# Kernel tuning notes

Measured on AMD Instinct MI355X. Metric: run time of the kernel, lower is better.

Reference implementation:

```python
import jax, jax.numpy as jnp
import numpy as np

# constants from init_kwargs
NUM_ITERS = 3
NUM_SLOTS = 8
INPUT_SIZE = 64
SLOT_SIZE = 64
MLP_HIDDEN = 128
EPS = 1e-8
NUM_HEADS = 4
HEAD_DIM = SLOT_SIZE // NUM_HEADS

B = 64
N_KV = 8192


def layernorm(x, g, b):
    m = jnp.mean(x, axis=-1, keepdims=True)
    v = jnp.mean((x - m) ** 2, axis=-1, keepdims=True)
    return (x - m) * jax.lax.rsqrt(v + 1e-5) * g + b


def setup_inputs() -> dict:
    key = jax.random.key(0)
    ks = jax.random.split(key, 16)
    s = 0.02
    return {
        "inputs": jax.random.normal(ks[0], (B, N_KV, INPUT_SIZE), jnp.float32),
        "slots": jax.random.normal(ks[1], (B, NUM_SLOTS, SLOT_SIZE), jnp.float32),
        "ln_in_g": jnp.ones((INPUT_SIZE,), jnp.float32),
        "ln_in_b": jnp.zeros((INPUT_SIZE,), jnp.float32),
        "ln_slot_g": jnp.ones((SLOT_SIZE,), jnp.float32),
        "ln_slot_b": jnp.zeros((SLOT_SIZE,), jnp.float32),
        "ln_mlp_g": jnp.ones((SLOT_SIZE,), jnp.float32),
        "ln_mlp_b": jnp.zeros((SLOT_SIZE,), jnp.float32),
        "Wq": jax.random.normal(ks[2], (SLOT_SIZE, SLOT_SIZE), jnp.float32) * s,
        "Wk": jax.random.normal(ks[3], (INPUT_SIZE, SLOT_SIZE), jnp.float32) * s,
        "Wv": jax.random.normal(ks[4], (INPUT_SIZE, SLOT_SIZE), jnp.float32) * s,
        "W_ih": jax.random.normal(ks[5], (3 * SLOT_SIZE, SLOT_SIZE), jnp.float32) * s,
        "W_hh": jax.random.normal(ks[6], (3 * SLOT_SIZE, SLOT_SIZE), jnp.float32) * s,
        "b_ih": jnp.zeros((3 * SLOT_SIZE,), jnp.float32),
        "b_hh": jnp.zeros((3 * SLOT_SIZE,), jnp.float32),
        "mlp_W1": jax.random.normal(ks[7], (SLOT_SIZE, MLP_HIDDEN), jnp.float32) * s,
        "mlp_b1": jnp.zeros((MLP_HIDDEN,), jnp.float32),
        "mlp_W2": jax.random.normal(ks[8], (MLP_HIDDEN, SLOT_SIZE), jnp.float32) * s,
        "mlp_b2": jnp.zeros((SLOT_SIZE,), jnp.float32),
    }


def gru_cell(x, h, W_ih, W_hh, b_ih, b_hh):
    # torch.nn.GRUCell math
    gx = x @ W_ih.T + b_ih  # [..., 3D]
    gh = h @ W_hh.T + b_hh
    xr, xz, xn = jnp.split(gx, 3, axis=-1)
    hr, hz, hn = jnp.split(gh, 3, axis=-1)
    r = jax.nn.sigmoid(xr + hr)
    z = jax.nn.sigmoid(xz + hz)
    n = jnp.tanh(xn + r * hn)
    return (1.0 - z) * n + z * h


def reference(inputs, slots, ln_in_g, ln_in_b, ln_slot_g, ln_slot_b, ln_mlp_g, ln_mlp_b,
              Wq, Wk, Wv, W_ih, W_hh, b_ih, b_hh, mlp_W1, mlp_b1, mlp_W2, mlp_b2):
    b, n_kv, _ = inputs.shape
    n_q = slots.shape[1]
    x = layernorm(inputs, ln_in_g, ln_in_b)
    k = (x @ Wk).reshape(b, n_kv, NUM_HEADS, HEAD_DIM).transpose(0, 2, 1, 3)  # [B,H,Nkv,Dh]
    v = (x @ Wv).reshape(b, n_kv, NUM_HEADS, HEAD_DIM).transpose(0, 2, 1, 3)
    k = k * (HEAD_DIM ** -0.5)
    attn_vis = None
    for _ in range(NUM_ITERS):
        slots_prev = slots
        s = layernorm(slots, ln_slot_g, ln_slot_b)
        q = (s @ Wq).reshape(b, n_q, NUM_HEADS, HEAD_DIM).transpose(0, 2, 1, 3)  # [B,H,Nq,Dh]
        logits = jnp.einsum('bhnd,bhqd->bhnq', k, q)  # [B,H,Nkv,Nq]
        # softmax jointly over (heads * slots) per kv token
        lt = logits.transpose(0, 2, 1, 3).reshape(b, n_kv, NUM_HEADS * n_q)
        attn = jax.nn.softmax(lt, axis=-1).reshape(b, n_kv, NUM_HEADS, n_q).transpose(0, 2, 1, 3)  # [B,H,Nkv,Nq]
        attn_vis = attn.sum(axis=1)  # [B,Nkv,Nq]
        attn = attn + EPS
        attn = attn / jnp.sum(attn, axis=-2, keepdims=True)  # normalize over Nkv
        updates = jnp.einsum('bhnq,bhnd->bqhd', attn, v).reshape(b, n_q, SLOT_SIZE)
        slots = gru_cell(updates, slots_prev, W_ih, W_hh, b_ih, b_hh)
        h = jax.nn.relu(layernorm(slots, ln_mlp_g, ln_mlp_b) @ mlp_W1 + mlp_b1)
        slots = slots + (h @ mlp_W2 + mlp_b2)
    return slots, attn_vis
```

## Files before the change

kernel.cpp:

```cpp
#include <hip/hip_runtime.h>

#define NKV 8192
#define NB 64

typedef __attribute__((ext_vector_type(8))) short short8;
typedef __attribute__((ext_vector_type(8))) unsigned short ushort8;
typedef __attribute__((ext_vector_type(4))) unsigned short usx4;
typedef __attribute__((ext_vector_type(4))) float f32x4;

__device__ __forceinline__ float bf2f(unsigned short u) {
  return __uint_as_float(((unsigned int)u) << 16);
}
__device__ __forceinline__ unsigned short f2bf(float f) {
  unsigned int x = __float_as_uint(f);
  return (unsigned short)((x + 0x7fffu + ((x >> 16) & 1u)) >> 16);
}
__device__ __forceinline__ float sigm(float x) { return 1.f / (1.f + __expf(-x)); }

__global__ __launch_bounds__(256) void k_wprep(
    const float* __restrict__ Wk, const float* __restrict__ Wv,
    unsigned short* __restrict__ wf) {
  int idx = blockIdx.x * 256 + threadIdx.x;
  int lane = idx & 63, ct = (idx >> 6) & 7, kf = idx >> 9;
  int half = lane >> 4, rlo = lane & 15;
  const float* W = (ct < 4) ? Wk : Wv;
  int cc = (ct & 3) * 16 + rlo;
  ushort8 pk;
#pragma unroll
  for (int i = 0; i < 8; ++i)
    pk[i] = f2bf(W[(kf * 32 + half * 8 + i) * 64 + cc]);
  *(ushort8*)(wf + (size_t)idx * 8) = pk;
}

__global__ __launch_bounds__(256) void k_proj(
    const float* __restrict__ x, const float* __restrict__ gin,
    const float* __restrict__ bin, const unsigned short* __restrict__ wf,
    unsigned short* __restrict__ kv) {
  const int lane = threadIdx.x & 63;
  const int wave = threadIdx.x >> 6;
  const int half = lane >> 4, rlo = lane & 15;

  short8 bfr[2][8];
  const ushort8* wf8 = (const ushort8*)wf;
#pragma unroll
  for (int kf = 0; kf < 2; ++kf)
#pragma unroll
    for (int ct = 0; ct < 8; ++ct)
      bfr[kf][ct] = (short8)wf8[(kf * 8 + ct) * 64 + lane];

  float g0[8], g1[8], bb0[8], bb1[8];
#pragma unroll
  for (int i = 0; i < 8; ++i) {
    g0[i] = gin[half * 8 + i];      bb0[i] = bin[half * 8 + i];
    g1[i] = gin[32 + half * 8 + i]; bb1[i] = bin[32 + half * 8 + i];
  }
  long tok0 = ((long)blockIdx.x * 4 + wave) * 128;
  for (int tile = 0; tile < 8; ++tile) {
    long row = tok0 + tile * 16 + rlo;
    const f32x4* p4 = (const f32x4*)(x + row * 64);
    f32x4 u0 = p4[half * 2], u1 = p4[half * 2 + 1];
    f32x4 u2 = p4[8 + half * 2], u3 = p4[9 + half * 2];
    float s = 0.f, ss = 0.f;
#pragma unroll
    for (int i = 0; i < 4; ++i) {
      s += u0[i] + u1[i] + u2[i] + u3[i];
      ss = fmaf(u0[i], u0[i], fmaf(u1[i], u1[i], fmaf(u2[i], u2[i], fmaf(u3[i], u3[i], ss))));
    }
    s += __shfl_xor(s, 16); ss += __shfl_xor(ss, 16);
    s += __shfl_xor(s, 32); ss += __shfl_xor(ss, 32);
    float m = s * 0.015625f;
    float var = ss * 0.015625f - m * m;
    float rs = rsqrtf(var + 1e-5f);
    short8 a0, a1;
#pragma unroll
    for (int i = 0; i < 4; ++i) {
      a0[i]     = (short)f2bf((u0[i] - m) * rs * g0[i]     + bb0[i]);
      a0[i + 4] = (short)f2bf((u1[i] - m) * rs * g0[i + 4] + bb0[i + 4]);
      a1[i]     = (short)f2bf((u2[i] - m) * rs * g1[i]     + bb1[i]);
      a1[i + 4] = (short)f2bf((u3[i] - m) * rs * g1[i + 4] + bb1[i + 4]);
    }
    long t = tok0 + tile * 16 + rlo;
#pragma unroll
    for (int ct = 0; ct < 8; ++ct) {
      f32x4 acc = {0.f, 0.f, 0.f, 0.f};
      acc = __builtin_amdgcn_mfma_f32_16x16x32_bf16(bfr[0][ct], a0, acc, 0, 0, 0);
      acc = __builtin_amdgcn_mfma_f32_16x16x32_bf16(bfr[1][ct], a1, acc, 0, 0, 0);
      float sc = (ct < 4) ? 0.25f : 1.f;
      usx4 pk;
#pragma unroll
      for (int r = 0; r < 4; ++r) pk[r] = f2bf(acc[r] * sc);
      *(usx4*)(kv + t * 128 + ct * 16 + half * 4) = pk;
    }
  }
}

__global__ __launch_bounds__(64) void k_prep(
    const float* __restrict__ slots_in, const float* __restrict__ g_slot,
    const float* __restrict__ b_slot, const float* __restrict__ Wq,
    float* __restrict__ slots_buf, float* __restrict__ qbuf,
    float* __restrict__ Sg, float* __restrict__ Wg) {
  int b = blockIdx.x >> 3, s = blockIdx.x & 7, d = threadIdx.x;
  __shared__ float l2_s[64];
  float x = slots_in[(b * 8 + s) * 64 + d];
  slots_buf[(b * 8 + s) * 64 + d] = x;
  float sum = x, sq = x * x;
#pragma unroll
  for (int msk = 1; msk < 64; msk <<= 1) { sum += __shfl_xor(sum, msk); sq += __shfl_xor(sq, msk); }
  float mean = sum * 0.015625f, var = sq * 0.015625f - mean * mean;
  float ln = (x - mean) * rsqrtf(var + 1e-5f) * g_slot[d] + b_slot[d];
  l2_s[d] = ln;
  __syncthreads();
  float acc = 0.f;
#pragma unroll 8
  for (int j = 0; j < 64; ++j) acc = fmaf(l2_s[j], Wq[j * 64 + d], acc);
  acc *= 0.25f;
  int hh = d >> 4, dh = d & 15, hq = hh * 8 + s;
  qbuf[(b * 32 + hq) * 16 + dh] = acc;
  if (d < 4) Sg[b * 32 + d * 8 + s] = 0.f;
  Wg[(b * 32 + hq) * 16 + dh] = 0.f;
}

__global__ __launch_bounds__(256) void k_attn(
    const unsigned short* __restrict__ kv, const float* __restrict__ qbuf,
    float* __restrict__ Sg, float* __restrict__ Wg,
    float* __restrict__ vis, int last) {
  int b = blockIdx.x >> 5, chunk = blockIdx.x & 31;
  int lane = threadIdx.x & 63, wave = threadIdx.x >> 6;
  int hq = lane & 31, h = hq >> 3, qs = hq & 7;
  float qf[16];
  {
    const f32x4* qp = (const f32x4*)(qbuf + (b * 32 + hq) * 16);
#pragma unroll
    for (int i = 0; i < 4; ++i) {
      f32x4 t = qp[i];
      qf[i * 4 + 0] = t[0]; qf[i * 4 + 1] = t[1];
      qf[i * 4 + 2] = t[2]; qf[i * 4 + 3] = t[3];
    }
  }
  float Sl = 0.f, Wl[16];
#pragma unroll
  for (int d = 0; d < 16; ++d) Wl[d] = 0.f;
  int tb = chunk * 256 + wave * 64;
  for (int it = 0; it < 32; ++it) {
    int t = tb + it * 2 + (lane >> 5);
    long base = ((long)(b * NKV + t)) * 128;
    const ushort8* kp = (const ushort8*)(kv + base + h * 16);
    ushort8 k0 = kp[0], k1 = kp[1];
    const ushort8* vp = (const ushort8*)(kv + base + 64 + h * 16);
    ushort8 v0 = vp[0], v1 = vp[1];
    float logit = 0.f;
#pragma unroll
    for (int i = 0; i < 8; ++i) {
      logit = fmaf(bf2f(k0[i]), qf[i], logit);
      logit = fmaf(bf2f(k1[i]), qf[8 + i], logit);
    }
    float e = __expf(logit);
    float sum = e;
#pragma unroll
    for (int msk = 1; msk <= 16; msk <<= 1) sum += __shfl_xor(sum, msk);
    float attn = e * __builtin_amdgcn_rcpf(sum);
    if (last) {
      float vh = attn + __shfl_xor(attn, 8);
      vh += __shfl_xor(vh, 16);
      if (hq < 8) vis[((long)(b * NKV + t)) * 8 + qs] = vh;
    }
    Sl += attn;
#pragma unroll
    for (int i = 0; i < 8; ++i) {
      Wl[i]     = fmaf(attn, bf2f(v0[i]), Wl[i]);
      Wl[8 + i] = fmaf(attn, bf2f(v1[i]), Wl[8 + i]);
    }
  }
  Sl += __shfl_xor(Sl, 32);
#pragma unroll
  for (int d = 0; d < 16; ++d) Wl[d] += __shfl_xor(Wl[d], 32);
  __shared__ float redS[4][32];
  __shared__ float redW[4][32][16];
  if (lane < 32) {
    redS[wave][hq] = Sl;
#pragma unroll
    for (int d = 0; d < 16; ++d) redW[wave][hq][d] = Wl[d];
  }
  __syncthreads();
  int tid = threadIdx.x;
  if (tid < 32)
    atomicAdd(&Sg[b * 32 + tid],
              redS[0][tid] + redS[1][tid] + redS[2][tid] + redS[3][tid]);
#pragma unroll
  for (int r = 0; r < 2; ++r) {
    int idx = tid + r * 256;
    int hh = idx >> 4, dd = idx & 15;
    atomicAdd(&Wg[b * 512 + idx],
              redW[0][hh][dd] + redW[1][hh][dd] + redW[2][hh][dd] + redW[3][hh][dd]);
  }
}

__global__ __launch_bounds__(64) void k_update(
    float* __restrict__ Sg, float* __restrict__ Wg,
    float* __restrict__ slots_buf,
    const float* __restrict__ W_ih, const float* __restrict__ W_hh,
    const float* __restrict__ b_ih, const float* __restrict__ b_hh,
    const float* __restrict__ g_mlp, const float* __restrict__ b_mlp,
    const float* __restrict__ W1, const float* __restrict__ b1,
    const float* __restrict__ W2, const float* __restrict__ b2,
    const float* __restrict__ g_slot, const float* __restrict__ b_slot,
    const float* __restrict__ Wq, float* __restrict__ qbuf,
    float* __restrict__ out_slots, int compute_next, int write_out) {
  int b = blockIdx.x >> 3, s = blockIdx.x & 7, d = threadIdx.x;
  __shared__ float upd_s[64], h_s[64], lnm_s[64], h1_s[128], l2_s[64];
  float hp = slots_buf[(b * 8 + s) * 64 + d];
  int hh = d >> 4, dh = d & 15, hq = hh * 8 + s;
  float denom = Sg[b * 32 + hq] + 8192.f * 1e-8f;
  float updv = Wg[(b * 32 + hq) * 16 + dh] / denom;
  upd_s[d] = updv; h_s[d] = hp;
  __syncthreads();
  float xr = b_ih[d], xz = b_ih[64 + d], xn = b_ih[128 + d];
  float hr = b_hh[d], hz = b_hh[64 + d], hv3 = b_hh[128 + d];
  const float* wi0 = W_ih + d * 64;
  const float* wi1 = W_ih + (64 + d) * 64;
  const float* wi2 = W_ih + (128 + d) * 64;
  const float* wh0 = W_hh + d * 64;
  const float* wh1 = W_hh + (64 + d) * 64;
  const float* wh2 = W_hh + (128 + d) * 64;
#pragma unroll 4
  for (int jj = 0; jj < 16; ++jj) {
    f32x4 u = *(const f32x4*)&upd_s[jj * 4];
    f32x4 hvv = *(const f32x4*)&h_s[jj * 4];
    f32x4 a0 = *(const f32x4*)&wi0[jj * 4];
    f32x4 a1 = *(const f32x4*)&wi1[jj * 4];
    f32x4 a2 = *(const f32x4*)&wi2[jj * 4];
    f32x4 c0 = *(const f32x4*)&wh0[jj * 4];
    f32x4 c1 = *(const f32x4*)&wh1[jj * 4];
    f32x4 c2 = *(const f32x4*)&wh2[jj * 4];
#pragma unroll
    for (int i = 0; i < 4; ++i) {
      xr = fmaf(u[i], a0[i], xr);  xz = fmaf(u[i], a1[i], xz);  xn = fmaf(u[i], a2[i], xn);
      hr = fmaf(hvv[i], c0[i], hr); hz = fmaf(hvv[i], c1[i], hz); hv3 = fmaf(hvv[i], c2[i], hv3);
    }
  }
  float r = sigm(xr + hr);
  float z = sigm(xz + hz);
  float n = tanhf(xn + r * hv3);
  float hn = (1.f - z) * n + z * hp;
  float sum = hn, sq = hn * hn;
#pragma unroll
  for (int msk = 1; msk < 64; msk <<= 1) { sum += __shfl_xor(sum, msk); sq += __shfl_xor(sq, msk); }
  float mean = sum * 0.015625f, var = sq * 0.015625f - mean * mean;
  float lnv = (hn - mean) * rsqrtf(var + 1e-5f) * g_mlp[d] + b_mlp[d];
  lnm_s[d] = lnv;
  __syncthreads();
  float a1a = b1[d], a1b = b1[64 + d];
#pragma unroll 8
  for (int j = 0; j < 64; ++j) {
    float lj = lnm_s[j];
    a1a = fmaf(lj, W1[j * 128 + d], a1a);
    a1b = fmaf(lj, W1[j * 128 + 64 + d], a1b);
  }
  h1_s[d] = fmaxf(a1a, 0.f); h1_s[64 + d] = fmaxf(a1b, 0.f);
  __syncthreads();
  float a2 = b2[d];
#pragma unroll 8
  for (int c = 0; c < 128; ++c) a2 = fmaf(h1_s[c], W2[c * 64 + d], a2);
  float outv = hn + a2;
  slots_buf[(b * 8 + s) * 64 + d] = outv;
  if (write_out) out_slots[(b * 8 + s) * 64 + d] = outv;
  if (compute_next) {
    float sum2 = outv, sq2 = outv * outv;
#pragma unroll
    for (int msk = 1; msk < 64; msk <<= 1) { sum2 += __shfl_xor(sum2, msk); sq2 += __shfl_xor(sq2, msk); }
    float mean2 = sum2 * 0.015625f, var2 = sq2 * 0.015625f - mean2 * mean2;
    float l2 = (outv - mean2) * rsqrtf(var2 + 1e-5f) * g_slot[d] + b_slot[d];
    l2_s[d] = l2;
    __syncthreads();
    float acc = 0.f;
#pragma unroll 8
    for (int j = 0; j < 64; ++j) acc = fmaf(l2_s[j], Wq[j * 64 + d], acc);
    acc *= 0.25f;
    qbuf[(b * 32 + hq) * 16 + dh] = acc;
    if (d < 4) Sg[b * 32 + d * 8 + s] = 0.f;
    Wg[(b * 32 + hq) * 16 + dh] = 0.f;
  }
}

extern "C" void kernel_launch(void* const* d_in, const int* in_sizes, int n_in,
                              void* d_out, int out_size, void* d_ws, size_t ws_size,
                              hipStream_t stream) {
  const float* inputs    = (const float*)d_in[0];
  const float* slots     = (const float*)d_in[1];
  const float* ln_in_g   = (const float*)d_in[2];
  const float* ln_in_b   = (const float*)d_in[3];
  const float* ln_slot_g = (const float*)d_in[4];
  const float* ln_slot_b = (const float*)d_in[5];
  const float* ln_mlp_g  = (const float*)d_in[6];
  const float* ln_mlp_b  = (const float*)d_in[7];
  const float* Wq        = (const float*)d_in[8];
  const float* Wk        = (const float*)d_in[9];
  const float* Wv        = (const float*)d_in[10];
  const float* W_ih      = (const float*)d_in[11];
  const float* W_hh      = (const float*)d_in[12];
  const float* b_ih      = (const float*)d_in[13];
  const float* b_hh      = (const float*)d_in[14];
  const float* mlp_W1    = (const float*)d_in[15];
  const float* mlp_b1    = (const float*)d_in[16];
  const float* mlp_W2    = (const float*)d_in[17];
  const float* mlp_b2    = (const float*)d_in[18];

  float* out_slots = (float*)d_out;
  float* out_vis   = out_slots + 64 * 8 * 64;

  char* ws = (char*)d_ws;
  unsigned short* kv = (unsigned short*)ws;
  size_t off = (size_t)64 * 8192 * 128 * 2;
  float* qbuf      = (float*)(ws + off); off += (size_t)64 * 32 * 16 * 4;
  float* Sg        = (float*)(ws + off); off += (size_t)64 * 32 * 4;
  float* Wg        = (float*)(ws + off); off += (size_t)64 * 512 * 4;
  float* slots_buf = (float*)(ws + off); off += (size_t)64 * 512 * 4;
  unsigned short* wf = (unsigned short*)(ws + off); off += (size_t)1024 * 8 * 2;

  hipLaunchKernelGGL(k_wprep, dim3(4), dim3(256), 0, stream, Wk, Wv, wf);
  hipLaunchKernelGGL(k_proj, dim3(1024), dim3(256), 0, stream,
                     inputs, ln_in_g, ln_in_b, wf, kv);
  hipLaunchKernelGGL(k_prep, dim3(512), dim3(64), 0, stream,
                     slots, ln_slot_g, ln_slot_b, Wq, slots_buf, qbuf, Sg, Wg);
  for (int it = 0; it < 3; ++it) {
    hipLaunchKernelGGL(k_attn, dim3(64 * 32), dim3(256), 0, stream,
                       kv, qbuf, Sg, Wg, out_vis, it == 2 ? 1 : 0);
    hipLaunchKernelGGL(k_update, dim3(512), dim3(64), 0, stream,
                       Sg, Wg, slots_buf, W_ih, W_hh, b_ih, b_hh,
                       ln_mlp_g, ln_mlp_b, mlp_W1, mlp_b1, mlp_W2, mlp_b2,
                       ln_slot_g, ln_slot_b, Wq, qbuf, out_slots,
                       it < 2 ? 1 : 0, it == 2 ? 1 : 0);
  }
}
```

Before: 484.2 us.

## Compute slot-attention logits and weighted values with bf16 MFMA

Measured after the change: 467.7 us. 1.04x faster.

```diff
diff --git a/kernel.cpp b/kernel.cpp
--- a/kernel.cpp
+++ b/kernel.cpp
@@ -120,81 +120,149 @@
   Wg[(b * 32 + hq) * 16 + dh] = 0.f;
 }
 
+__global__ __launch_bounds__(64) void k_qfrag(
+    const float* __restrict__ qbuf, unsigned short* __restrict__ qfrag) {
+  int b = blockIdx.x, lane = threadIdx.x;
+  int half = lane >> 4, rlo = lane & 15;
+#pragma unroll
+  for (int m = 0; m < 2; ++m) {
+    int hq = m * 16 + rlo, h = hq >> 3;
+#pragma unroll
+    for (int kc = 0; kc < 2; ++kc) {
+      ushort8 pk;
+#pragma unroll
+      for (int i = 0; i < 8; ++i) {
+        int d = kc * 32 + half * 8 + i;
+        float v = ((d >> 4) == h) ? qbuf[(b * 32 + hq) * 16 + (d & 15)] : 0.f;
+        pk[i] = f2bf(v);
+      }
+      *(ushort8*)(qfrag + ((size_t)(b * 4 + m * 2 + kc) * 64 + lane) * 8) = pk;
+    }
+  }
+}
+
+template <int IT>
 __global__ __launch_bounds__(256) void k_attn(
-    const unsigned short* __restrict__ kv, const float* __restrict__ qbuf,
+    const unsigned short* __restrict__ kv, const unsigned short* __restrict__ qfrag,
     float* __restrict__ Sg, float* __restrict__ Wg,
-    float* __restrict__ vis, int last) {
+    float* __restrict__ vis) {
+  constexpr bool last = (IT == 2);
+  const int PS = 34;
   int b = blockIdx.x >> 5, chunk = blockIdx.x & 31;
   int lane = threadIdx.x & 63, wave = threadIdx.x >> 6;
-  int hq = lane & 31, h = hq >> 3, qs = hq & 7;
-  float qf[16];
-  {
-    const f32x4* qp = (const f32x4*)(qbuf + (b * 32 + hq) * 16);
-#pragma unroll
-    for (int i = 0; i < 4; ++i) {
-      f32x4 t = qp[i];
-      qf[i * 4 + 0] = t[0]; qf[i * 4 + 1] = t[1];
-      qf[i * 4 + 2] = t[2]; qf[i * 4 + 3] = t[3];
-    }
-  }
-  float Sl = 0.f, Wl[16];
-#pragma unroll
-  for (int d = 0; d < 16; ++d) Wl[d] = 0.f;
-  int tb = chunk * 256 + wave * 64;
-  for (int it = 0; it < 32; ++it) {
-    int t = tb + it * 2 + (lane >> 5);
-    long base = ((long)(b * NKV + t)) * 128;
-    const ushort8* kp = (const ushort8*)(kv + base + h * 16);
-    ushort8 k0 = kp[0], k1 = kp[1];
-    const ushort8* vp = (const ushort8*)(kv + base + 64 + h * 16);
-    ushort8 v0 = vp[0], v1 = vp[1];
-    float logit = 0.f;
-#pragma unroll
-    for (int i = 0; i < 8; ++i) {
-      logit = fmaf(bf2f(k0[i]), qf[i], logit);
-      logit = fmaf(bf2f(k1[i]), qf[8 + i], logit);
-    }
-    float e = __expf(logit);
-    float sum = e;
-#pragma unroll
-    for (int msk = 1; msk <= 16; msk <<= 1) sum += __shfl_xor(sum, msk);
-    float attn = e * __builtin_amdgcn_rcpf(sum);
+  int half = lane >> 4, rlo = lane & 15;
+  __shared__ unsigned short P[4][64 * PS];
+  __shared__ float Wred[4][512];
+  int t0 = chunk * 256 + wave * 64;
+
+  short8 afr[2][2];
+  const ushort8* qf8 = (const ushort8*)qfrag;
+#pragma unroll
+  for (int m = 0; m < 2; ++m)
+#pragma unroll
+    for (int kc = 0; kc < 2; ++kc)
+      afr[m][kc] = (short8)qf8[(b * 4 + m * 2 + kc) * 64 + lane];
+
+  float Sacc[2][4];
+#pragma unroll
+  for (int m = 0; m < 2; ++m)
+#pragma unroll
+    for (int r = 0; r < 4; ++r) Sacc[m][r] = 0.f;
+
+#pragma unroll
+  for (int nt = 0; nt < 4; ++nt) {
+    long rowb = ((long)(b * NKV) + t0 + nt * 16 + rlo) * 128;
+    short8 bk0 = *(const short8*)(kv + rowb + half * 8);
+    short8 bk1 = *(const short8*)(kv + rowb + 32 + half * 8);
+    f32x4 acc0 = {0.f, 0.f, 0.f, 0.f}, acc1 = {0.f, 0.f, 0.f, 0.f};
+    acc0 = __builtin_amdgcn_mfma_f32_16x16x32_bf16(afr[0][0], bk0, acc0, 0, 0, 0);
+    acc0 = __builtin_amdgcn_mfma_f32_16x16x32_bf16(afr[0][1], bk1, acc0, 0, 0, 0);
+    acc1 = __builtin_amdgcn_mfma_f32_16x16x32_bf16(afr[1][0], bk0, acc1, 0, 0, 0);
+    acc1 = __builtin_amdgcn_mfma_f32_16x16x32_bf16(afr[1][1], bk1, acc1, 0, 0, 0);
+    float e0[4], e1[4], ssum = 0.f;
+#pragma unroll
+    for (int r = 0; r < 4; ++r) {
+      e0[r] = __expf(acc0[r]); e1[r] = __expf(acc1[r]);
+      ssum += e0[r] + e1[r];
+    }
+    ssum += __shfl_xor(ssum, 16);
+    ssum += __shfl_xor(ssum, 32);
+    float rs = __builtin_amdgcn_rcpf(ssum);
+    float a0[4], a1[4];
+#pragma unroll
+    for (int r = 0; r < 4; ++r) {
+      a0[r] = e0[r] * rs; a1[r] = e1[r] * rs;
+      Sacc[0][r] += a0[r]; Sacc[1][r] += a1[r];
+    }
+    int off = (nt * 16 + rlo) * PS;
+    unsigned int w00 = (unsigned int)f2bf(a0[0]) | ((unsigned int)f2bf(a0[1]) << 16);
+    unsigned int w01 = (unsigned int)f2bf(a0[2]) | ((unsigned int)f2bf(a0[3]) << 16);
+    unsigned int w10 = (unsigned int)f2bf(a1[0]) | ((unsigned int)f2bf(a1[1]) << 16);
+    unsigned int w11 = (unsigned int)f2bf(a1[2]) | ((unsigned int)f2bf(a1[3]) << 16);
+    *(unsigned int*)(&P[wave][off + half * 4])      = w00;
+    *(unsigned int*)(&P[wave][off + half * 4 + 2])  = w01;
+    *(unsigned int*)(&P[wave][off + 16 + half * 4]) = w10;
+    *(unsigned int*)(&P[wave][off + 16 + half * 4 + 2]) = w11;
     if (last) {
-      float vh = attn + __shfl_xor(attn, 8);
-      vh += __shfl_xor(vh, 16);
-      if (hq < 8) vis[((long)(b * NKV + t)) * 8 + qs] = vh;
-    }
-    Sl += attn;
-#pragma unroll
-    for (int i = 0; i < 8; ++i) {
-      Wl[i]     = fmaf(attn, bf2f(v0[i]), Wl[i]);
-      Wl[8 + i] = fmaf(attn, bf2f(v1[i]), Wl[8 + i]);
-    }
-  }
-  Sl += __shfl_xor(Sl, 32);
-#pragma unroll
-  for (int d = 0; d < 16; ++d) Wl[d] += __shfl_xor(Wl[d], 32);
-  __shared__ float redS[4][32];
-  __shared__ float redW[4][32][16];
-  if (lane < 32) {
-    redS[wave][hq] = Sl;
-#pragma unroll
-    for (int d = 0; d < 16; ++d) redW[wave][hq][d] = Wl[d];
+      float vl[4];
+#pragma unroll
+      for (int r = 0; r < 4; ++r) {
+        vl[r] = a0[r] + a1[r];
+        vl[r] += __shfl_xor(vl[r], 32);
+      }
+      if (half < 2) {
+        long tt = (long)b * NKV + t0 + nt * 16 + rlo;
+#pragma unroll
+        for (int r = 0; r < 4; ++r) vis[tt * 8 + (half & 1) * 4 + r] = vl[r];
+      }
+    }
+  }
+#pragma unroll
+  for (int m = 0; m < 2; ++m)
+#pragma unroll
+    for (int r = 0; r < 4; ++r) {
+      Sacc[m][r] += __shfl_xor(Sacc[m][r], 1);
+      Sacc[m][r] += __shfl_xor(Sacc[m][r], 2);
+      Sacc[m][r] += __shfl_xor(Sacc[m][r], 4);
+      Sacc[m][r] += __shfl_xor(Sacc[m][r], 8);
+    }
+  if (rlo == 0) {
+#pragma unroll
+    for (int m = 0; m < 2; ++m)
+#pragma unroll
+      for (int r = 0; r < 4; ++r)
+        atomicAdd(&Sg[b * 32 + m * 16 + half * 4 + r], Sacc[m][r]);
+  }
+#pragma unroll
+  for (int h = 0; h < 4; ++h) {
+    f32x4 wacc = {0.f, 0.f, 0.f, 0.f};
+#pragma unroll
+    for (int kc2 = 0; kc2 < 2; ++kc2) {
+      short8 af, bf;
+#pragma unroll
+      for (int i = 0; i < 8; ++i) {
+        af[i] = (short)P[wave][(kc2 * 32 + half * 8 + i) * PS + h * 8 + (rlo & 7)];
+        bf[i] = (short)kv[((long)(b * NKV) + t0 + kc2 * 32 + half * 8 + i) * 128 + 64 + h * 16 + rlo];
+      }
+      wacc = __builtin_amdgcn_mfma_f32_16x16x32_bf16(af, bf, wacc, 0, 0, 0);
+    }
+    if (half < 2) {
+#pragma unroll
+      for (int r = 0; r < 4; ++r)
+        Wred[wave][(h * 8 + half * 4 + r) * 16 + rlo] = wacc[r];
+    }
   }
   __syncthreads();
   int tid = threadIdx.x;
-  if (tid < 32)
-    atomicAdd(&Sg[b * 32 + tid],
-              redS[0][tid] + redS[1][tid] + redS[2][tid] + redS[3][tid]);
-#pragma unroll
-  for (int r = 0; r < 2; ++r) {
-    int idx = tid + r * 256;
-    int hh = idx >> 4, dd = idx & 15;
+#pragma unroll
+  for (int r2 = 0; r2 < 2; ++r2) {
+    int idx = tid + r2 * 256;
     atomicAdd(&Wg[b * 512 + idx],
-              redW[0][hh][dd] + redW[1][hh][dd] + redW[2][hh][dd] + redW[3][hh][dd]);
-  }
-}
-
+              Wred[0][idx] + Wred[1][idx] + Wred[2][idx] + Wred[3][idx]);
+  }
+}
+
+template <int IT>
 __global__ __launch_bounds__(64) void k_update(
     float* __restrict__ Sg, float* __restrict__ Wg,
     float* __restrict__ slots_buf,
@@ -205,7 +273,9 @@
     const float* __restrict__ W2, const float* __restrict__ b2,
     const float* __restrict__ g_slot, const float* __restrict__ b_slot,
     const float* __restrict__ Wq, float* __restrict__ qbuf,
-    float* __restrict__ out_slots, int compute_next, int write_out) {
+    float* __restrict__ out_slots) {
+  constexpr int compute_next = (IT < 2);
+  constexpr int write_out = (IT == 2);
   int b = blockIdx.x >> 3, s = blockIdx.x & 7, d = threadIdx.x;
   __shared__ float upd_s[64], h_s[64], lnm_s[64], h1_s[128], l2_s[64];
   float hp = slots_buf[(b * 8 + s) * 64 + d];
@@ -316,19 +386,33 @@
   float* Wg        = (float*)(ws + off); off += (size_t)64 * 512 * 4;
   float* slots_buf = (float*)(ws + off); off += (size_t)64 * 512 * 4;
   unsigned short* wf = (unsigned short*)(ws + off); off += (size_t)1024 * 8 * 2;
+  unsigned short* qfrag = (unsigned short*)(ws + off); off += (size_t)64 * 4 * 64 * 8 * 2;
 
   hipLaunchKernelGGL(k_wprep, dim3(4), dim3(256), 0, stream, Wk, Wv, wf);
   hipLaunchKernelGGL(k_proj, dim3(1024), dim3(256), 0, stream,
                      inputs, ln_in_g, ln_in_b, wf, kv);
   hipLaunchKernelGGL(k_prep, dim3(512), dim3(64), 0, stream,
                      slots, ln_slot_g, ln_slot_b, Wq, slots_buf, qbuf, Sg, Wg);
-  for (int it = 0; it < 3; ++it) {
-    hipLaunchKernelGGL(k_attn, dim3(64 * 32), dim3(256), 0, stream,
-                       kv, qbuf, Sg, Wg, out_vis, it == 2 ? 1 : 0);
-    hipLaunchKernelGGL(k_update, dim3(512), dim3(64), 0, stream,
-                       Sg, Wg, slots_buf, W_ih, W_hh, b_ih, b_hh,
-                       ln_mlp_g, ln_mlp_b, mlp_W1, mlp_b1, mlp_W2, mlp_b2,
-                       ln_slot_g, ln_slot_b, Wq, qbuf, out_slots,
-                       it < 2 ? 1 : 0, it == 2 ? 1 : 0);
-  }
-}
+  hipLaunchKernelGGL(k_qfrag, dim3(64), dim3(64), 0, stream, qbuf, qfrag);
+
+  hipLaunchKernelGGL((k_attn<0>), dim3(64 * 32), dim3(256), 0, stream,
+                     kv, qfrag, Sg, Wg, out_vis);
+  hipLaunchKernelGGL((k_update<0>), dim3(512), dim3(64), 0, stream,
+                     Sg, Wg, slots_buf, W_ih, W_hh, b_ih, b_hh,
+                     ln_mlp_g, ln_mlp_b, mlp_W1, mlp_b1, mlp_W2, mlp_b2,
+                     ln_slot_g, ln_slot_b, Wq, qbuf, out_slots);
+  hipLaunchKernelGGL(k_qfrag, dim3(64), dim3(64), 0, stream, qbuf, qfrag);
+  hipLaunchKernelGGL((k_attn<1>), dim3(64 * 32), dim3(256), 0, stream,
+                     kv, qfrag, Sg, Wg, out_vis);
+  hipLaunchKernelGGL((k_update<1>), dim3(512), dim3(64), 0, stream,
+                     Sg, Wg, slots_buf, W_ih, W_hh, b_ih, b_hh,
+                     ln_mlp_g, ln_mlp_b, mlp_W1, mlp_b1, mlp_W2, mlp_b2,
+                     ln_slot_g, ln_slot_b, Wq, qbuf, out_slots);
+  hipLaunchKernelGGL(k_qfrag, dim3(64), dim3(64), 0, stream, qbuf, qfrag);
+  hipLaunchKernelGGL((k_attn<2>), dim3(64 * 32), dim3(256), 0, stream,
+                     kv, qfrag, Sg, Wg, out_vis);
+  hipLaunchKernelGGL((k_update<2>), dim3(512), dim3(64), 0, stream,
+                     Sg, Wg, slots_buf, W_ih, W_hh, b_ih, b_hh,
+                     ln_mlp_g, ln_mlp_b, mlp_W1, mlp_b1, mlp_W2, mlp_b2,
+                     ln_slot_g, ln_slot_b, Wq, qbuf, out_slots);
+}
```
